# Kernel tuning notes

Measured on AMD Instinct MI355X. Metric: run time of the kernel, lower is better.

## Reference

```python
import jax, jax.numpy as jnp
import numpy as np

B, T, D, N = 4, 2048, 1024, 16

def setup_inputs() -> dict:
    key = jax.random.key(0)
    ks = jax.random.split(key, 6)
    scale = 0.02
    return {
        'x': jax.random.normal(ks[0], (B, T, D), dtype=jnp.float32),
        'Wd': jax.random.normal(ks[1], (D, D), dtype=jnp.float32) * (1.0 / np.sqrt(D)),
        'bd': jnp.zeros((D,), dtype=jnp.float32),
        'a_log': jax.random.normal(ks[2], (D, N), dtype=jnp.float32) * scale,
        'b_param': jax.random.normal(ks[3], (D, N), dtype=jnp.float32) * scale,
        'Wo': jax.random.normal(ks[4], (D, D), dtype=jnp.float32) * (1.0 / np.sqrt(D)),
        'bo': jnp.zeros((D,), dtype=jnp.float32),
    }

def reference(x, Wd, bd, a_log, b_param, Wo, bo):
    # delta: [B,T,D]
    delta = jax.nn.softplus(jnp.einsum('btd,ed->bte', x, Wd) + bd)
    a_pos = jax.nn.softplus(a_log) + 1e-4  # [D,N]

    def step(state, inputs):
        x_t, delta_t = inputs  # [B,D], [B,D]
        dt = delta_t[..., None]                      # [B,D,1]
        a_bar = jnp.exp(-dt * a_pos)                 # [B,D,N]
        state = a_bar * state + (dt * b_param) * x_t[..., None]
        return state, state.sum(axis=-1)             # y_t: [B,D]

    init = jnp.zeros((B, D, N), dtype=x.dtype)
    xs = (jnp.swapaxes(x, 0, 1), jnp.swapaxes(delta, 0, 1))  # [T,B,D]
    _, y = jax.lax.scan(step, init, xs)              # y: [T,B,D]
    y = jnp.swapaxes(y, 0, 1)                        # [B,T,D]
    return jnp.einsum('btd,ed->bte', y, Wo) + bo
```

## Files before the change

kernel.cpp:

```cpp
#include <hip/hip_runtime.h>
#include <hip/hip_bf16.h>

#define B_ 4
#define T_ 2048
#define D_ 1024
#define N_ 16
#define TCH 32
#define NCH 64

#define GM 8192
#define GK 1024
#define GN 1024

typedef __attribute__((ext_vector_type(4))) float f32x4;
typedef __attribute__((ext_vector_type(8))) short short8;
typedef unsigned int u32;
typedef unsigned short u16;

#if defined(__has_builtin)
#if __has_builtin(__builtin_amdgcn_exp2f)
#define EXP2(x) __builtin_amdgcn_exp2f(x)
#else
#define EXP2(x) exp2f(x)
#endif
#else
#define EXP2(x) exp2f(x)
#endif

__device__ __forceinline__ float softplus_f(float v) {
    return v > 20.f ? v : log1pf(__expf(v));
}

__device__ __forceinline__ u16 f2bf(float f) {
    u32 u = __float_as_uint(f);
    u32 r = (u + 0x7fffu + ((u >> 16) & 1u)) >> 16;
    return (u16)r;
}
__device__ __forceinline__ float bf2f(u16 v) {
    return __uint_as_float(((u32)v) << 16);
}

#define NX4 (GM * GK / 4)
#define NW4 (GK * GN / 4)
__global__ __launch_bounds__(256) void cvt_all(const float* __restrict__ x,
                                               const float* __restrict__ Wd,
                                               const float* __restrict__ Wo,
                                               u16* __restrict__ xbf,
                                               u16* __restrict__ wdbf,
                                               u16* __restrict__ wobf) {
    const int i = blockIdx.x * 256 + threadIdx.x;
    const float* src; u16* dst; int j;
    if (i < NX4)            { src = x;  dst = xbf;  j = i; }
    else if (i < NX4 + NW4) { src = Wd; dst = wdbf; j = i - NX4; }
    else                    { src = Wo; dst = wobf; j = i - NX4 - NW4; }
    float4 v = ((const float4*)src)[j];
    ushort4 o;
    o.x = f2bf(v.x); o.y = f2bf(v.y); o.z = f2bf(v.z); o.w = f2bf(v.w);
    ((ushort4*)dst)[j] = o;
}

template <int ACT, int OBF>
__global__ __launch_bounds__(512, 8) void gemm_bt(const u16* __restrict__ A,
                                                  const u16* __restrict__ Bw,
                                                  const float* __restrict__ bias,
                                                  void* __restrict__ Cout) {
    __shared__ __align__(16) u16 sA[64 * 64];
    __shared__ __align__(16) u16 sB[128 * 64];
    const int tid = threadIdx.x;
    const int wid = tid >> 6;
    const int lane = tid & 63;

    const int wg = blockIdx.x;
    const int xcd = wg & 7;
    const int jj = wg >> 3;
    const int bx = xcd * 16 + (jj & 15);
    const int by = jj >> 4;
    const int m0 = bx * 64;
    const int n0 = by * 128;
    const int wm = wid >> 2;
    const int wn = wid & 3;

    const int lrow = lane >> 3;
    const int slot = lane & 7;
    const int ksw = (slot ^ lrow) << 3;

    const u16* aP  = A  + (size_t)(m0 + wid * 8 + lrow) * GK + ksw;
    const u16* bP0 = Bw + (size_t)(n0 + wid * 8 + lrow) * GK + ksw;
    const u16* bP1 = Bw + (size_t)(n0 + (wid + 8) * 8 + lrow) * GK + ksw;

    const int wOff = wid * 1024 + lrow * 128 + slot * 16;
    char* const wA  = (char*)sA + wOff;
    char* const wB  = (char*)sB + wOff;

    const int fr = lane & 15;
    const int g = lane >> 4;
    const int xorv = (fr & 7) << 4;
    const char* const rA0 = (const char*)sA + (wm * 32 + fr) * 128 + ((g * 16) ^ xorv);
    const char* const rA1 = (const char*)sA + (wm * 32 + fr) * 128 + ((64 + g * 16) ^ xorv);
    const char* const rB0 = (const char*)sB + (wn * 32 + fr) * 128 + ((g * 16) ^ xorv);
    const char* const rB1 = (const char*)sB + (wn * 32 + fr) * 128 + ((64 + g * 16) ^ xorv);

    short8 ra, rb0, rb1;
    f32x4 acc[2][2] = {};

    ra  = *(const short8*)(aP);
    rb0 = *(const short8*)(bP0);
    rb1 = *(const short8*)(bP1);
    *(short8*)(wA)        = ra;
    *(short8*)(wB)        = rb0;
    *(short8*)(wB + 8192) = rb1;
    ra  = *(const short8*)(aP + 64);
    rb0 = *(const short8*)(bP0 + 64);
    rb1 = *(const short8*)(bP1 + 64);
    asm volatile("s_waitcnt lgkmcnt(0)" ::: "memory");
    __builtin_amdgcn_s_barrier();
    asm volatile("" ::: "memory");

    #pragma unroll
    for (int t = 0; t < GK / 64; ++t) {
        #pragma unroll
        for (int kk = 0; kk < 2; ++kk) {
            const char* bA = kk ? rA1 : rA0;
            const char* bB = kk ? rB1 : rB0;
            short8 af[2], bf[2];
            #pragma unroll
            for (int f = 0; f < 2; ++f)
                af[f] = *(const short8*)(bA + f * 2048);
            #pragma unroll
            for (int f = 0; f < 2; ++f)
                bf[f] = *(const short8*)(bB + f * 2048);
            __builtin_amdgcn_s_setprio(1);
            #pragma unroll
            for (int i = 0; i < 2; ++i)
                #pragma unroll
                for (int j2 = 0; j2 < 2; ++j2)
                    acc[i][j2] = __builtin_amdgcn_mfma_f32_16x16x32_bf16(af[i], bf[j2],
                                                                         acc[i][j2], 0, 0, 0);
            __builtin_amdgcn_s_setprio(0);
        }
        if (t + 1 < GK / 64) {
            asm volatile("s_waitcnt lgkmcnt(0)" ::: "memory");
            __builtin_amdgcn_s_barrier();
            asm volatile("" ::: "memory");
            *(short8*)(wA)        = ra;
            *(short8*)(wB)        = rb0;
            *(short8*)(wB + 8192) = rb1;
            asm volatile("s_waitcnt lgkmcnt(0)" ::: "memory");
            __builtin_amdgcn_s_barrier();
            asm volatile("" ::: "memory");
            if (t + 2 < GK / 64) {
                ra  = *(const short8*)(aP  + (t + 2) * 64);
                rb0 = *(const short8*)(bP0 + (t + 2) * 64);
                rb1 = *(const short8*)(bP1 + (t + 2) * 64);
            }
        }
    }

    const int cl = lane & 15;
    const int rg = (lane >> 4) * 4;
    #pragma unroll
    for (int j2 = 0; j2 < 2; ++j2) {
        const int col = n0 + wn * 32 + j2 * 16 + cl;
        const float bv = bias[col];
        #pragma unroll
        for (int i = 0; i < 2; ++i) {
            #pragma unroll
            for (int r = 0; r < 4; ++r) {
                const int rowg = m0 + wm * 32 + i * 16 + rg + r;
                float v = acc[i][j2][r] + bv;
                if (ACT) v = softplus_f(v);
                if (OBF) ((u16*)Cout)[(size_t)rowg * GN + col] = f2bf(v);
                else     ((float*)Cout)[(size_t)rowg * GN + col] = v;
            }
        }
    }
}

__global__ __launch_bounds__(256) void scan_p1(const u16* __restrict__ delta,
                                               const u16* __restrict__ x,
                                               const float* __restrict__ a_log,
                                               float* __restrict__ S,
                                               float* __restrict__ dtsum) {
    const int gid = blockIdx.x * 256 + threadIdx.x;
    const int lane = gid & 63;
    const int w = gid >> 6;
    const int dw = w & 31;
    const int cb = w >> 5;
    const int d = dw * 32 + (lane & 31);
    const int half = lane >> 5;
    const int b = cb & (B_ - 1);
    const int c = cb >> 2;

    float an2[8];
    {
        const float4* a4 = (const float4*)&a_log[d * N_ + half * 8];
        float4 a0 = a4[0], a1 = a4[1];
        an2[0] = (softplus_f(a0.x) + 1e-4f) * 1.44269504f;
        an2[1] = (softplus_f(a0.y) + 1e-4f) * 1.44269504f;
        an2[2] = (softplus_f(a0.z) + 1e-4f) * 1.44269504f;
        an2[3] = (softplus_f(a0.w) + 1e-4f) * 1.44269504f;
        an2[4] = (softplus_f(a1.x) + 1e-4f) * 1.44269504f;
        an2[5] = (softplus_f(a1.y) + 1e-4f) * 1.44269504f;
        an2[6] = (softplus_f(a1.z) + 1e-4f) * 1.44269504f;
        an2[7] = (softplus_f(a1.w) + 1e-4f) * 1.44269504f;
    }

    float s[8];
    #pragma unroll
    for (int n = 0; n < 8; ++n) s[n] = 0.f;
    float dts = 0.f;

    const size_t base = ((size_t)b * T_ + (size_t)c * TCH) * D_ + d;
    float dt = bf2f(delta[base]);
    float xv = bf2f(x[base]);
    for (int i = 0; i < TCH; ++i) {
        float dtn = 0.f, xvn = 0.f;
        if (i + 1 < TCH) {
            dtn = bf2f(delta[base + (size_t)(i + 1) * D_]);
            xvn = bf2f(x[base + (size_t)(i + 1) * D_]);
        }
        const float dtx = dt * xv;
        dts += dt;
        #pragma unroll
        for (int n = 0; n < 8; ++n) {
            const float ab = EXP2(-dt * an2[n]);
            s[n] = fmaf(ab, s[n], dtx);
        }
        dt = dtn; xv = xvn;
    }

    float4* So = (float4*)&S[((size_t)cb * D_ + d) * N_ + half * 8];
    So[0] = make_float4(s[0], s[1], s[2], s[3]);
    So[1] = make_float4(s[4], s[5], s[6], s[7]);
    if (half == 0) dtsum[(size_t)cb * D_ + d] = dts;
}

__global__ __launch_bounds__(256) void scan_p2(const float* __restrict__ S,
                                               const float* __restrict__ dtsum,
                                               const float* __restrict__ a_log,
                                               float* __restrict__ carry_out) {
    const int gid = blockIdx.x * 256 + threadIdx.x;
    const int n = gid & 15;
    const int d = (gid >> 4) & (D_ - 1);
    const int b = gid >> 14;
    const float an2 = (softplus_f(a_log[d * N_ + n]) + 1e-4f) * 1.44269504f;
    float carry = 0.f;
    #pragma unroll 8
    for (int c = 0; c < NCH; ++c) {
        const size_t cb = (size_t)c * B_ + b;
        const size_t idx = (cb * D_ + d) * N_ + n;
        carry_out[idx] = carry;
        const float dts = dtsum[cb * D_ + d];
        const float P = EXP2(-dts * an2);
        carry = fmaf(P, carry, S[idx]);
    }
}

__global__ __launch_bounds__(256) void scan_p3(const u16* __restrict__ delta,
                                               const u16* __restrict__ x,
                                               const float* __restrict__ a_log,
                                               const float* __restrict__ b_param,
                                               const float* __restrict__ carry_in,
                                               u16* __restrict__ y) {
    const int gid = blockIdx.x * 256 + threadIdx.x;
    const int lane = gid & 63;
    const int w = gid >> 6;
    const int dw = w & 31;
    const int cb = w >> 5;
    const int d = dw * 32 + (lane & 31);
    const int half = lane >> 5;
    const int b = cb & (B_ - 1);
    const int c = cb >> 2;

    float an2[8], bp[8];
    {
        const float4* a4 = (const float4*)&a_log[d * N_ + half * 8];
        const float4* b4 = (const float4*)&b_param[d * N_ + half * 8];
        float4 a0 = a4[0], a1 = a4[1];
        float4 v0 = b4[0], v1 = b4[1];
        an2[0] = (softplus_f(a0.x) + 1e-4f) * 1.44269504f;
        an2[1] = (softplus_f(a0.y) + 1e-4f) * 1.44269504f;
        an2[2] = (softplus_f(a0.z) + 1e-4f) * 1.44269504f;
        an2[3] = (softplus_f(a0.w) + 1e-4f) * 1.44269504f;
        an2[4] = (softplus_f(a1.x) + 1e-4f) * 1.44269504f;
        an2[5] = (softplus_f(a1.y) + 1e-4f) * 1.44269504f;
        an2[6] = (softplus_f(a1.z) + 1e-4f) * 1.44269504f;
        an2[7] = (softplus_f(a1.w) + 1e-4f) * 1.44269504f;
        bp[0] = v0.x; bp[1] = v0.y; bp[2] = v0.z; bp[3] = v0.w;
        bp[4] = v1.x; bp[5] = v1.y; bp[6] = v1.z; bp[7] = v1.w;
    }

    float s[8];
    {
        const float4* ci = (const float4*)&carry_in[((size_t)cb * D_ + d) * N_ + half * 8];
        float4 c0 = ci[0], c1 = ci[1];
        s[0] = c0.x; s[1] = c0.y; s[2] = c0.z; s[3] = c0.w;
        s[4] = c1.x; s[5] = c1.y; s[6] = c1.z; s[7] = c1.w;
    }

    const size_t base = ((size_t)b * T_ + (size_t)c * TCH) * D_ + d;
    float dt = bf2f(delta[base]);
    float xv = bf2f(x[base]);
    for (int i = 0; i < TCH; ++i) {
        float dtn = 0.f, xvn = 0.f;
        if (i + 1 < TCH) {
            dtn = bf2f(delta[base + (size_t)(i + 1) * D_]);
            xvn = bf2f(x[base + (size_t)(i + 1) * D_]);
        }
        const float dtx = dt * xv;
        float acc = 0.f;
        #pragma unroll
        for (int n = 0; n < 8; ++n) {
            const float ab = EXP2(-dt * an2[n]);
            s[n] = fmaf(ab, s[n], dtx);
            acc = fmaf(bp[n], s[n], acc);
        }
        const float tot = acc + __shfl_xor(acc, 32);
        if (half == 0) y[base + (size_t)i * D_] = f2bf(tot);
        dt = dtn; xv = xvn;
    }
}

extern "C" void kernel_launch(void* const* d_in, const int* in_sizes, int n_in,
                              void* d_out, int out_size, void* d_ws, size_t ws_size,
                              hipStream_t stream) {
    const float* x      = (const float*)d_in[0];
    const float* Wd     = (const float*)d_in[1];
    const float* bd     = (const float*)d_in[2];
    const float* a_log  = (const float*)d_in[3];
    const float* b_par  = (const float*)d_in[4];
    const float* Wo     = (const float*)d_in[5];
    const float* bo     = (const float*)d_in[6];
    float* out = (float*)d_out;

    char* ws = (char*)d_ws;
    u16*   xbf     = (u16*)(ws);
    float* S       = (float*)(ws + 16777216);
    u16*   ybf     = (u16*)(ws + 16777216);
    u16*   deltabf = (u16*)(ws + 33554432);
    float* carry   = (float*)(ws + 50331648);
    u16*   wdbf    = (u16*)(ws + 67108864);
    u16*   wobf    = (u16*)(ws + 69206016);
    float* dtsum   = (float*)(ws + 71303168);
    (void)in_sizes; (void)n_in; (void)out_size; (void)ws_size;

    cvt_all<<<(NX4 + 2 * NW4) / 256, 256, 0, stream>>>(x, Wd, Wo, xbf, wdbf, wobf);

    gemm_bt<1, 1><<<(GM / 64) * (GN / 128), 512, 0, stream>>>(xbf, wdbf, bd, deltabf);

    scan_p1<<<NCH * B_ * D_ * 2 / 256, 256, 0, stream>>>(deltabf, xbf, a_log, S, dtsum);
    scan_p2<<<B_ * D_ * N_ / 256, 256, 0, stream>>>(S, dtsum, a_log, carry);
    scan_p3<<<NCH * B_ * D_ * 2 / 256, 256, 0, stream>>>(deltabf, xbf, a_log, b_par, carry, ybf);

    gemm_bt<0, 0><<<(GM / 64) * (GN / 128), 512, 0, stream>>>(ybf, wobf, bo, out);
}
```

Before: 163.7 us.

## Fuse three-phase chunked scan into one cooperative kernel with grid syncs

```diff
diff --git a/kernel.cpp b/kernel.cpp
--- a/kernel.cpp
+++ b/kernel.cpp
@@ -1,5 +1,6 @@
 #include <hip/hip_runtime.h>
 #include <hip/hip_bf16.h>
+#include <hip/hip_cooperative_groups.h>
 
 #define B_ 4
 #define T_ 2048
@@ -321,6 +322,160 @@
     }
 }
 
+#define CUNITS (NCH * B_ * D_ * 2)
+#define CSTRIDE (CUNITS / 2)
+__global__ __launch_bounds__(256, 8) void scan_fused(const u16* __restrict__ delta,
+                                                     const u16* __restrict__ x,
+                                                     const float* __restrict__ a_log,
+                                                     const float* __restrict__ b_param,
+                                                     float* __restrict__ S,
+                                                     float* __restrict__ dtsum,
+                                                     float* __restrict__ carry,
+                                                     u16* __restrict__ y) {
+    cooperative_groups::grid_group grid = cooperative_groups::this_grid();
+    const int tid0 = blockIdx.x * 256 + threadIdx.x;
+
+    #pragma unroll
+    for (int u = 0; u < 2; ++u) {
+        const int gid = tid0 + u * CSTRIDE;
+        const int lane = gid & 63;
+        const int w = gid >> 6;
+        const int dw = w & 31;
+        const int cb = w >> 5;
+        const int d = dw * 32 + (lane & 31);
+        const int half = lane >> 5;
+        const int b = cb & (B_ - 1);
+        const int c = cb >> 2;
+
+        float an2[8];
+        {
+            const float4* a4 = (const float4*)&a_log[d * N_ + half * 8];
+            float4 a0 = a4[0], a1 = a4[1];
+            an2[0] = (softplus_f(a0.x) + 1e-4f) * 1.44269504f;
+            an2[1] = (softplus_f(a0.y) + 1e-4f) * 1.44269504f;
+            an2[2] = (softplus_f(a0.z) + 1e-4f) * 1.44269504f;
+            an2[3] = (softplus_f(a0.w) + 1e-4f) * 1.44269504f;
+            an2[4] = (softplus_f(a1.x) + 1e-4f) * 1.44269504f;
+            an2[5] = (softplus_f(a1.y) + 1e-4f) * 1.44269504f;
+            an2[6] = (softplus_f(a1.z) + 1e-4f) * 1.44269504f;
+            an2[7] = (softplus_f(a1.w) + 1e-4f) * 1.44269504f;
+        }
+
+        float s[8];
+        #pragma unroll
+        for (int n = 0; n < 8; ++n) s[n] = 0.f;
+        float dts = 0.f;
+
+        const size_t base = ((size_t)b * T_ + (size_t)c * TCH) * D_ + d;
+        float dt = bf2f(delta[base]);
+        float xv = bf2f(x[base]);
+        for (int i = 0; i < TCH; ++i) {
+            float dtn = 0.f, xvn = 0.f;
+            if (i + 1 < TCH) {
+                dtn = bf2f(delta[base + (size_t)(i + 1) * D_]);
+                xvn = bf2f(x[base + (size_t)(i + 1) * D_]);
+            }
+            const float dtx = dt * xv;
+            dts += dt;
+            #pragma unroll
+            for (int n = 0; n < 8; ++n) {
+                const float ab = EXP2(-dt * an2[n]);
+                s[n] = fmaf(ab, s[n], dtx);
+            }
+            dt = dtn; xv = xvn;
+        }
+
+        float4* So = (float4*)&S[((size_t)cb * D_ + d) * N_ + half * 8];
+        So[0] = make_float4(s[0], s[1], s[2], s[3]);
+        So[1] = make_float4(s[4], s[5], s[6], s[7]);
+        if (half == 0) dtsum[(size_t)cb * D_ + d] = dts;
+    }
+
+    __threadfence();
+    grid.sync();
+
+    if (blockIdx.x < 256) {
+        const int g2 = tid0;
+        const int n2 = g2 & 15;
+        const int d2 = (g2 >> 4) & (D_ - 1);
+        const int b2 = g2 >> 14;
+        const float a2 = (softplus_f(a_log[d2 * N_ + n2]) + 1e-4f) * 1.44269504f;
+        float cy = 0.f;
+        #pragma unroll 8
+        for (int c2 = 0; c2 < NCH; ++c2) {
+            const size_t cb2 = (size_t)c2 * B_ + b2;
+            const size_t idx = (cb2 * D_ + d2) * N_ + n2;
+            carry[idx] = cy;
+            const float dts = dtsum[cb2 * D_ + d2];
+            const float P = EXP2(-dts * a2);
+            cy = fmaf(P, cy, S[idx]);
+        }
+    }
+
+    __threadfence();
+    grid.sync();
+
+    #pragma unroll
+    for (int u = 0; u < 2; ++u) {
+        const int gid = tid0 + u * CSTRIDE;
+        const int lane = gid & 63;
+        const int w = gid >> 6;
+        const int dw = w & 31;
+        const int cb = w >> 5;
+        const int d = dw * 32 + (lane & 31);
+        const int half = lane >> 5;
+        const int b = cb & (B_ - 1);
+        const int c = cb >> 2;
+
+        float an2[8], bp[8];
+        {
+            const float4* a4 = (const float4*)&a_log[d * N_ + half * 8];
+            const float4* b4 = (const float4*)&b_param[d * N_ + half * 8];
+            float4 a0 = a4[0], a1 = a4[1];
+            float4 v0 = b4[0], v1 = b4[1];
+            an2[0] = (softplus_f(a0.x) + 1e-4f) * 1.44269504f;
+            an2[1] = (softplus_f(a0.y) + 1e-4f) * 1.44269504f;
+            an2[2] = (softplus_f(a0.z) + 1e-4f) * 1.44269504f;
+            an2[3] = (softplus_f(a0.w) + 1e-4f) * 1.44269504f;
+            an2[4] = (softplus_f(a1.x) + 1e-4f) * 1.44269504f;
+            an2[5] = (softplus_f(a1.y) + 1e-4f) * 1.44269504f;
+            an2[6] = (softplus_f(a1.z) + 1e-4f) * 1.44269504f;
+            an2[7] = (softplus_f(a1.w) + 1e-4f) * 1.44269504f;
+            bp[0] = v0.x; bp[1] = v0.y; bp[2] = v0.z; bp[3] = v0.w;
+            bp[4] = v1.x; bp[5] = v1.y; bp[6] = v1.z; bp[7] = v1.w;
+        }
+        float s[8];
+        {
+            const float4* ci = (const float4*)&carry[((size_t)cb * D_ + d) * N_ + half * 8];
+            float4 c0 = ci[0], c1 = ci[1];
+            s[0] = c0.x; s[1] = c0.y; s[2] = c0.z; s[3] = c0.w;
+            s[4] = c1.x; s[5] = c1.y; s[6] = c1.z; s[7] = c1.w;
+        }
+
+        const size_t base = ((size_t)b * T_ + (size_t)c * TCH) * D_ + d;
+        float dt = bf2f(delta[base]);
+        float xv = bf2f(x[base]);
+        for (int i = 0; i < TCH; ++i) {
+            float dtn = 0.f, xvn = 0.f;
+            if (i + 1 < TCH) {
+                dtn = bf2f(delta[base + (size_t)(i + 1) * D_]);
+                xvn = bf2f(x[base + (size_t)(i + 1) * D_]);
+            }
+            const float dtx = dt * xv;
+            float acc = 0.f;
+            #pragma unroll
+            for (int n = 0; n < 8; ++n) {
+                const float ab = EXP2(-dt * an2[n]);
+                s[n] = fmaf(ab, s[n], dtx);
+                acc = fmaf(bp[n], s[n], acc);
+            }
+            const float tot = acc + __shfl_xor(acc, 32);
+            if (half == 0) y[base + (size_t)i * D_] = f2bf(tot);
+            dt = dtn; xv = xvn;
+        }
+    }
+}
+
 extern "C" void kernel_launch(void* const* d_in, const int* in_sizes, int n_in,
                               void* d_out, int out_size, void* d_ws, size_t ws_size,
                               hipStream_t stream) {
@@ -348,9 +503,18 @@
 
     gemm_bt<1, 1><<<(GM / 64) * (GN / 128), 512, 0, stream>>>(xbf, wdbf, bd, deltabf);
 
-    scan_p1<<<NCH * B_ * D_ * 2 / 256, 256, 0, stream>>>(deltabf, xbf, a_log, S, dtsum);
-    scan_p2<<<B_ * D_ * N_ / 256, 256, 0, stream>>>(S, dtsum, a_log, carry);
-    scan_p3<<<NCH * B_ * D_ * 2 / 256, 256, 0, stream>>>(deltabf, xbf, a_log, b_par, carry, ybf);
+    {
+        void* args[] = { (void*)&deltabf, (void*)&xbf, (void*)&a_log, (void*)&b_par,
+                         (void*)&S, (void*)&dtsum, (void*)&carry, (void*)&ybf };
+        hipError_t e = hipLaunchCooperativeKernel((void*)scan_fused,
+                                                  dim3(CSTRIDE / 256), dim3(256),
+                                                  args, 0, stream);
+        if (e != hipSuccess) {
+            scan_p1<<<CUNITS / 256, 256, 0, stream>>>(deltabf, xbf, a_log, S, dtsum);
+            scan_p2<<<B_ * D_ * N_ / 256, 256, 0, stream>>>(S, dtsum, a_log, carry);
+            scan_p3<<<CUNITS / 256, 256, 0, stream>>>(deltabf, xbf, a_log, b_par, carry, ybf);
+        }
+    }
 
     gemm_bt<0, 0><<<(GM / 64) * (GN / 128), 512, 0, stream>>>(ybf, wobf, bo, out);
 }
```

New measurement: 574.6 us. 251% more time.
